# Performance work log

Hardware: AMD Instinct MI355X
Metric: run time of the kernel (lower is better)

## Reference

```python
import jax, jax.numpy as jnp
import numpy as np

IN_FEATURES = 4096
OUT_FEATURES = 4096


def setup_inputs() -> dict:
    key = jax.random.key(0)
    k_x, k_w, k_b = jax.random.split(key, 3)
    inp = {
        "input": jax.random.normal(k_x, (4, 2048, IN_FEATURES), dtype=jnp.float32),
        # learned int8 weight table [out_features, in_features]
        "weight_int8": jax.random.randint(k_w, (OUT_FEATURES, IN_FEATURES), -128, 128, dtype=jnp.int32).astype(jnp.int8),
        # per-tensor dequant scales (scalars, as in the module buffers)
        "scale": jnp.asarray(0.01, dtype=jnp.float32),
        "x_scale": jnp.asarray(0.05, dtype=jnp.float32),
        "bias": jax.random.normal(k_b, (OUT_FEATURES,), dtype=jnp.float32) * 0.02,
    }
    return inp


def reference(input, weight_int8, scale, x_scale, bias):
    # --- quantize activations per-tensor to int8 (W8A8 path) ---
    x_int8 = jnp.clip(jnp.round(input / x_scale), -128, 127).astype(jnp.int8)
    in_shape = input.shape
    x_flat = x_int8.reshape(-1, in_shape[-1])  # [B*S, in]
    # contract x_flat[k] with weight_int8[n, k] -> [B*S, out]
    out_i32 = jax.lax.dot_general(
        x_flat, weight_int8,
        dimension_numbers=(((1,), (1,)), ((), ())),
        preferred_element_type=jnp.int32,
    )
    # --- dequant epilogue: combined scale, reshape, bias ---
    out = out_i32.astype(input.dtype) * (scale * x_scale)
    out = out.reshape(*in_shape[:-1], weight_int8.shape[0])
    out = out + bias
    return out
```

## Files before the change

### kernel.cpp

```cpp
#include <hip/hip_runtime.h>

#define KDIM 4096
#define NDIM 4096
#define BM 256
#define BN 256
#define BK 128
#define NTILE (KDIM / BK)
#define BBUF 32768

using i32x4 = __attribute__((ext_vector_type(4))) int;

__device__ __forceinline__ void g2l16(const void* g, void* l) {
  __builtin_amdgcn_global_load_lds(
      (const __attribute__((address_space(1))) void*)g,
      (__attribute__((address_space(3))) void*)l,
      16, 0, 0);
}

__global__ void w8l_detect(const int* __restrict__ w32, int* __restrict__ flag) {
  __shared__ int s;
  const int t = threadIdx.x;
  if (t == 0) s = 1;
  __syncthreads();
  bool oob = false;
#pragma unroll
  for (int i = 0; i < 16; ++i) {
    int v = w32[t * 16 + i];
    if (v < -128 || v > 127) oob = true;
  }
  if (oob) atomicAnd(&s, 0);
  __syncthreads();
  if (t == 0) *flag = s;
}

__global__ void w8l_pack(const void* __restrict__ wsrc, const int* __restrict__ flag,
                         signed char* __restrict__ wq) {
  if (*flag == 0) return;
  const int t = blockIdx.x * blockDim.x + threadIdx.x;
  const int4* s = (const int4*)wsrc;
  int4 a = s[t * 4 + 0], b = s[t * 4 + 1], c = s[t * 4 + 2], d = s[t * 4 + 3];
  int4 o;
  o.x = (a.x & 255) | ((a.y & 255) << 8) | ((a.z & 255) << 16) | ((a.w & 255) << 24);
  o.y = (b.x & 255) | ((b.y & 255) << 8) | ((b.z & 255) << 16) | ((b.w & 255) << 24);
  o.z = (c.x & 255) | ((c.y & 255) << 8) | ((c.z & 255) << 16) | ((c.w & 255) << 24);
  o.w = (d.x & 255) | ((d.y & 255) << 8) | ((d.z & 255) << 16) | ((d.w & 255) << 24);
  ((int4*)wq)[t] = o;
}

__global__ void w8l_quant(const float* __restrict__ x, const float* __restrict__ xs,
                          signed char* __restrict__ aq) {
  const int t = blockIdx.x * blockDim.x + threadIdx.x;
  const float s = *xs;
  const int r = t & 15;
  const int kc = (t >> 4) & 255;
  const int mb = t >> 12;
  const float4* x4 = (const float4*)(x + (size_t)(mb * 16 + r) * KDIM + kc * 16);
  int4 o;
  int* op = (int*)&o;
#pragma unroll
  for (int q = 0; q < 4; ++q) {
    float4 f = x4[q];
    int v0 = __float2int_rn(f.x / s);
    int v1 = __float2int_rn(f.y / s);
    int v2 = __float2int_rn(f.z / s);
    int v3 = __float2int_rn(f.w / s);
    v0 = v0 < -128 ? -128 : (v0 > 127 ? 127 : v0);
    v1 = v1 < -128 ? -128 : (v1 > 127 ? 127 : v1);
    v2 = v2 < -128 ? -128 : (v2 > 127 ? 127 : v2);
    v3 = v3 < -128 ? -128 : (v3 > 127 ? 127 : v3);
    op[q] = (v0 & 255) | ((v1 & 255) << 8) | ((v2 & 255) << 16) | ((v3 & 255) << 24);
  }
  ((int4*)aq)[t] = o;
}

__global__ __launch_bounds__(512, 2) void w8l_gemm(
    const signed char* __restrict__ Ap,
    const signed char* __restrict__ Wraw, const signed char* __restrict__ Wpk,
    const int* __restrict__ flag,
    const float* __restrict__ scale, const float* __restrict__ xscale,
    const float* __restrict__ bias, float* __restrict__ out, int nbn) {
  __shared__ signed char lds[2 * BBUF];

  const signed char* __restrict__ Wq = (*flag) ? Wpk : Wraw;

  const int tid = threadIdx.x;
  const int lane = tid & 63;
  const int wid = tid >> 6;
  const int wr = wid >> 2;
  const int wc = wid & 3;
  const int l15 = lane & 15;
  const int l4 = (lane >> 4) & 3;

  const int nwg = gridDim.x;
  const int cpx = nwg >> 3;
  const int bid = blockIdx.x;
  const int swz = (bid & 7) * cpx + (bid >> 3);
  const int bm = swz / nbn, bn = swz % nbn;
  const int m0 = bm * BM, n0 = bn * BN;

  const unsigned r_in = (unsigned)tid >> 3;
  const unsigned c16 = (unsigned)tid & 7;
  const unsigned swcol = ((c16 ^ (r_in & 7u)) << 4);
  const signed char* wgp = Wq + (size_t)(n0 + r_in) * KDIM + swcol;
  const unsigned ldsoff = (unsigned)tid * 16u;

#define ISSUE_B(t)                                                           \
  do {                                                                       \
    const size_t koff_ = (size_t)(t) * BK;                                   \
    signed char* lb_ = lds + (unsigned)((t) & 1) * BBUF + ldsoff;            \
    _Pragma("unroll") for (int u = 0; u < 4; ++u)                            \
      g2l16(wgp + (size_t)(u * 64) * KDIM + koff_, lb_ + u * 8192);          \
  } while (0)

  const signed char* aglp =
      Ap + (size_t)(m0 / 16 + wr * 8) * 65536 + l4 * 256 + l15 * 16;

#define LOAD_A(dst, t, ks)                                                   \
  _Pragma("unroll") for (int mi = 0; mi < 8; ++mi)                           \
      dst[mi] = *(const i32x4*)(aglp + (size_t)mi * 65536 +                  \
                                (size_t)(t) * 2048 + (ks) * 1024);

  const unsigned b_lane = (unsigned)((wc * 64 + l15) * 128) +
                          (unsigned)((l4 ^ (l15 & 7)) << 4);

  i32x4 acc[8][4] = {};
  i32x4 aE[8], aO[8], b0[4], b1[4];

#define SB __builtin_amdgcn_sched_barrier(0)

  ISSUE_B(0);
  SB;
  LOAD_A(aE, 0, 0);
  SB;

#pragma unroll 1
  for (int kt = 0; kt < NTILE; ++kt) {
    asm volatile("s_waitcnt vmcnt(8)" ::: "memory");
    __builtin_amdgcn_s_barrier();
    SB;

    const signed char* Bb = lds + (unsigned)(kt & 1) * BBUF;
#pragma unroll
    for (int nj = 0; nj < 4; ++nj) {
      b0[nj] = *(const i32x4*)(Bb + (b_lane + nj * 2048));
      b1[nj] = *(const i32x4*)(Bb + ((b_lane + nj * 2048) ^ 64u));
    }
    SB;
    LOAD_A(aO, kt, 1);
    SB;
    if (kt + 1 < NTILE) ISSUE_B(kt + 1);
    SB;

    __builtin_amdgcn_s_setprio(1);
#pragma unroll
    for (int mi = 0; mi < 8; ++mi)
#pragma unroll
      for (int nj = 0; nj < 4; ++nj)
        acc[mi][nj] = __builtin_amdgcn_mfma_i32_16x16x64_i8(aE[mi], b0[nj], acc[mi][nj], 0, 0, 0);
    __builtin_amdgcn_s_setprio(0);
    SB;
    if (kt + 1 < NTILE) LOAD_A(aE, kt + 1, 0);
    SB;
    __builtin_amdgcn_s_setprio(1);
#pragma unroll
    for (int mi = 0; mi < 8; ++mi)
#pragma unroll
      for (int nj = 0; nj < 4; ++nj)
        acc[mi][nj] = __builtin_amdgcn_mfma_i32_16x16x64_i8(aO[mi], b1[nj], acc[mi][nj], 0, 0, 0);
    __builtin_amdgcn_s_setprio(0);
    SB;
  }

  const float cs = scale[0] * xscale[0];
#pragma unroll
  for (int nj = 0; nj < 4; ++nj) {
    const int n = n0 + wc * 64 + nj * 16 + l15;
    const float bj = bias[n];
#pragma unroll
    for (int mi = 0; mi < 8; ++mi) {
      const int m = m0 + wr * 128 + mi * 16 + l4 * 4;
      float* o = out + (size_t)m * NDIM + n;
#pragma unroll
      for (int v = 0; v < 4; ++v)
        o[(size_t)v * NDIM] = (float)acc[mi][nj][v] * cs + bj;
    }
  }
#undef ISSUE_B
#undef LOAD_A
#undef SB
}

extern "C" void kernel_launch(void* const* d_in, const int* in_sizes, int n_in,
                              void* d_out, int out_size, void* d_ws, size_t ws_size,
                              hipStream_t stream) {
  const float* x = (const float*)d_in[0];
  const void* w = d_in[1];
  const float* scale = (const float*)d_in[2];
  const float* xscale = (const float*)d_in[3];
  const float* bias = (const float*)d_in[4];
  float* out = (float*)d_out;

  const int M = in_sizes[0] / KDIM;

  int* flag = (int*)d_ws;
  signed char* wq = (signed char*)d_ws + 256;
  signed char* aq = wq + (size_t)NDIM * KDIM;

  const size_t need = 256 + (size_t)NDIM * KDIM + (size_t)M * KDIM;
  if (ws_size < need) return;

  w8l_detect<<<1, 256, 0, stream>>>((const int*)w, flag);
  w8l_pack<<<(NDIM * KDIM / 16) / 256, 256, 0, stream>>>(w, flag, wq);
  w8l_quant<<<(M * KDIM / 16) / 256, 256, 0, stream>>>(x, xscale, aq);

  const int nbn = NDIM / BN;
  w8l_gemm<<<(M / BM) * nbn, 512, 0, stream>>>(
      aq, (const signed char*)w, wq, flag, scale, xscale, bias, out, nbn);
}
```

Measured before the change: 201.7 us.

## Switch GEMM to 32x32x32 MFMA with 4 waves and triple-buffered LDS

Rewrites the int8 GEMM main loop to use 4 waves of 128x128 per-wave tiles with 32x32x32 i8 MFMA instead of 8 waves using 16x16x64. The B tile is now triple-buffered in LDS with a new XOR swizzle and prefetched two tiles ahead, and the loop is unrolled by two to alternate A register sets. The aim is more data reuse per wave and fewer LDS reads per MFMA. The cost is much higher register pressure with 64 accumulator VGPRs per tile set, only one workgroup per CU, and a full vmcnt(0) wait each iteration.

```diff
diff --git a/kernel.cpp b/kernel.cpp
--- a/kernel.cpp
+++ b/kernel.cpp
@@ -9,6 +9,7 @@
 #define BBUF 32768
 
 using i32x4 = __attribute__((ext_vector_type(4))) int;
+using i32x16 = __attribute__((ext_vector_type(16))) int;
 
 __device__ __forceinline__ void g2l16(const void* g, void* l) {
   __builtin_amdgcn_global_load_lds(
@@ -73,23 +74,23 @@
   ((int4*)aq)[t] = o;
 }
 
-__global__ __launch_bounds__(512, 2) void w8l_gemm(
+__global__ __launch_bounds__(256, 1) void w8l_gemm(
     const signed char* __restrict__ Ap,
     const signed char* __restrict__ Wraw, const signed char* __restrict__ Wpk,
     const int* __restrict__ flag,
     const float* __restrict__ scale, const float* __restrict__ xscale,
     const float* __restrict__ bias, float* __restrict__ out, int nbn) {
-  __shared__ signed char lds[2 * BBUF];
+  __shared__ signed char lds[3 * BBUF];
 
   const signed char* __restrict__ Wq = (*flag) ? Wpk : Wraw;
 
   const int tid = threadIdx.x;
   const int lane = tid & 63;
   const int wid = tid >> 6;
-  const int wr = wid >> 2;
-  const int wc = wid & 3;
-  const int l15 = lane & 15;
-  const int l4 = (lane >> 4) & 3;
+  const int wr = wid >> 1;
+  const int wc = wid & 1;
+  const int l31 = lane & 31;
+  const int l5 = lane >> 5;
 
   const int nwg = gridDim.x;
   const int cpx = nwg >> 3;
@@ -100,93 +101,110 @@
 
   const unsigned r_in = (unsigned)tid >> 3;
   const unsigned c16 = (unsigned)tid & 7;
-  const unsigned swcol = ((c16 ^ (r_in & 7u)) << 4);
-  const signed char* wgp = Wq + (size_t)(n0 + r_in) * KDIM + swcol;
+  const unsigned s_r = (r_in ^ (r_in >> 3)) & 7u;
+  const signed char* wgp0 = Wq + (size_t)(n0 + r_in) * KDIM + ((c16 ^ s_r) << 4);
+  const signed char* wgp1 = Wq + (size_t)(n0 + r_in) * KDIM + ((c16 ^ s_r ^ 4u) << 4);
   const unsigned ldsoff = (unsigned)tid * 16u;
 
-#define ISSUE_B(t)                                                           \
-  do {                                                                       \
-    const size_t koff_ = (size_t)(t) * BK;                                   \
-    signed char* lb_ = lds + (unsigned)((t) & 1) * BBUF + ldsoff;            \
-    _Pragma("unroll") for (int u = 0; u < 4; ++u)                            \
-      g2l16(wgp + (size_t)(u * 64) * KDIM + koff_, lb_ + u * 8192);          \
+#define ISSUE_B(t, buf)                                                       \
+  do {                                                                        \
+    const size_t koff_ = (size_t)(t) * BK;                                    \
+    signed char* lb_ = lds + (unsigned)(buf) * (unsigned)BBUF + ldsoff;       \
+    _Pragma("unroll") for (int u = 0; u < 8; ++u) {                           \
+      const signed char* gp_ = (u & 1) ? wgp1 : wgp0;                         \
+      g2l16(gp_ + (size_t)(u * 32) * KDIM + koff_, lb_ + u * 4096);           \
+    }                                                                         \
   } while (0)
 
-  const signed char* aglp =
-      Ap + (size_t)(m0 / 16 + wr * 8) * 65536 + l4 * 256 + l15 * 16;
-
-#define LOAD_A(dst, t, ks)                                                   \
-  _Pragma("unroll") for (int mi = 0; mi < 8; ++mi)                           \
-      dst[mi] = *(const i32x4*)(aglp + (size_t)mi * 65536 +                  \
-                                (size_t)(t) * 2048 + (ks) * 1024);
-
-  const unsigned b_lane = (unsigned)((wc * 64 + l15) * 128) +
-                          (unsigned)((l4 ^ (l15 & 7)) << 4);
-
-  i32x4 acc[8][4] = {};
-  i32x4 aE[8], aO[8], b0[4], b1[4];
+  const signed char* aglp = Ap +
+      (size_t)((m0 >> 4) + wr * 8 + (l31 >> 4)) * 65536 +
+      (size_t)l5 * 256 + (size_t)(l31 & 15) * 16;
+
+#define LOAD_A(dst, t)                                                        \
+  _Pragma("unroll") for (int ks = 0; ks < 4; ++ks)                            \
+      _Pragma("unroll") for (int mi = 0; mi < 4; ++mi)                        \
+          dst[ks][mi] = *(const i32x4*)(aglp + (size_t)mi * 131072 +          \
+                                        (size_t)(t) * 2048 + ks * 512);
+
+#define RD_B(dst, base, ks)                                                   \
+  _Pragma("unroll") for (int nj = 0; nj < 4; ++nj) {                          \
+    const int r_ = wc * 128 + nj * 32 + l31;                                  \
+    const int sx_ = (r_ ^ (r_ >> 3)) & 7;                                     \
+    dst[nj] = *(const i32x4*)((base) + r_ * 128 +                             \
+                              ((((ks) * 2 + l5) ^ sx_) << 4));                \
+  }
 
 #define SB __builtin_amdgcn_sched_barrier(0)
 
-  ISSUE_B(0);
+#define MFMA16(a4, b4)                                                        \
+  __builtin_amdgcn_s_setprio(1);                                              \
+  _Pragma("unroll") for (int mi = 0; mi < 4; ++mi)                            \
+      _Pragma("unroll") for (int nj = 0; nj < 4; ++nj)                        \
+          acc[mi][nj] = __builtin_amdgcn_mfma_i32_32x32x32_i8(                \
+              a4[mi], b4[nj], acc[mi][nj], 0, 0, 0);                          \
+  __builtin_amdgcn_s_setprio(0);
+
+  i32x16 acc[4][4] = {};
+  i32x4 aE[4][4], aO[4][4], b0[4], b1[4], b2[4];
+
+#define BODY(t, AC, AN)                                                       \
+  do {                                                                        \
+    asm volatile("s_waitcnt vmcnt(0)" ::: "memory");  \
+    __builtin_amdgcn_s_barrier();                                             \
+    SB;                                                                       \
+    if ((t) + 2 < NTILE) ISSUE_B((t) + 2, ((t) + 2) % 3);                     \
+    SB;                                                                       \
+    if ((t) + 1 < NTILE) LOAD_A(AN, (t) + 1);                                 \
+    SB;                                                                       \
+    const signed char* base_ = lds + (unsigned)((t) % 3) * (unsigned)BBUF;    \
+    RD_B(b0, base_, 0);                                                       \
+    RD_B(b1, base_, 1);                                                       \
+    RD_B(b2, base_, 2);                                                       \
+    SB;                                                                       \
+    MFMA16(AC[0], b0);                                                        \
+    SB;                                                                       \
+    RD_B(b0, base_, 3);      \
+    SB;                                                                       \
+    MFMA16(AC[1], b1);                                                        \
+    SB;                                                                       \
+    MFMA16(AC[2], b2);                                                        \
+    SB;                                                                       \
+    MFMA16(AC[3], b0);                                                        \
+    SB;                                                                       \
+  } while (0)
+
+  ISSUE_B(0, 0);
+  ISSUE_B(1, 1);
   SB;
-  LOAD_A(aE, 0, 0);
+  LOAD_A(aE, 0);
   SB;
 
 #pragma unroll 1
-  for (int kt = 0; kt < NTILE; ++kt) {
-    asm volatile("s_waitcnt vmcnt(8)" ::: "memory");
-    __builtin_amdgcn_s_barrier();
-    SB;
-
-    const signed char* Bb = lds + (unsigned)(kt & 1) * BBUF;
-#pragma unroll
-    for (int nj = 0; nj < 4; ++nj) {
-      b0[nj] = *(const i32x4*)(Bb + (b_lane + nj * 2048));
-      b1[nj] = *(const i32x4*)(Bb + ((b_lane + nj * 2048) ^ 64u));
-    }
-    SB;
-    LOAD_A(aO, kt, 1);
-    SB;
-    if (kt + 1 < NTILE) ISSUE_B(kt + 1);
-    SB;
-
-    __builtin_amdgcn_s_setprio(1);
-#pragma unroll
-    for (int mi = 0; mi < 8; ++mi)
-#pragma unroll
-      for (int nj = 0; nj < 4; ++nj)
-        acc[mi][nj] = __builtin_amdgcn_mfma_i32_16x16x64_i8(aE[mi], b0[nj], acc[mi][nj], 0, 0, 0);
-    __builtin_amdgcn_s_setprio(0);
-    SB;
-    if (kt + 1 < NTILE) LOAD_A(aE, kt + 1, 0);
-    SB;
-    __builtin_amdgcn_s_setprio(1);
-#pragma unroll
-    for (int mi = 0; mi < 8; ++mi)
-#pragma unroll
-      for (int nj = 0; nj < 4; ++nj)
-        acc[mi][nj] = __builtin_amdgcn_mfma_i32_16x16x64_i8(aO[mi], b1[nj], acc[mi][nj], 0, 0, 0);
-    __builtin_amdgcn_s_setprio(0);
-    SB;
+  for (int kt = 0; kt < NTILE; kt += 2) {
+    BODY(kt, aE, aO);
+    BODY(kt + 1, aO, aE);
   }
 
   const float cs = scale[0] * xscale[0];
 #pragma unroll
   for (int nj = 0; nj < 4; ++nj) {
-    const int n = n0 + wc * 64 + nj * 16 + l15;
+    const int n = n0 + wc * 128 + nj * 32 + l31;
     const float bj = bias[n];
 #pragma unroll
-    for (int mi = 0; mi < 8; ++mi) {
-      const int m = m0 + wr * 128 + mi * 16 + l4 * 4;
-      float* o = out + (size_t)m * NDIM + n;
-#pragma unroll
-      for (int v = 0; v < 4; ++v)
-        o[(size_t)v * NDIM] = (float)acc[mi][nj][v] * cs + bj;
+    for (int mi = 0; mi < 4; ++mi) {
+      const int mbase = m0 + wr * 128 + mi * 32 + l5 * 4;
+#pragma unroll
+      for (int r = 0; r < 16; ++r) {
+        const int m = mbase + (r & 3) + 8 * (r >> 2);
+        out[(size_t)m * NDIM + n] = (float)acc[mi][nj][r] * cs + bj;
+      }
     }
   }
 #undef ISSUE_B
 #undef LOAD_A
+#undef RD_B
+#undef MFMA16
+#undef BODY
 #undef SB
 }
 
@@ -214,6 +232,6 @@
   w8l_quant<<<(M * KDIM / 16) / 256, 256, 0, stream>>>(x, xscale, aq);
 
   const int nbn = NDIM / BN;
-  w8l_gemm<<<(M / BM) * nbn, 512, 0, stream>>>(
+  w8l_gemm<<<(M / BM) * nbn, 256, 0, stream>>>(
       aq, (const signed char*)w, wq, flag, scale, xscale, bias, out, nbn);
 }
```

Result: slower. 340.2 us (+68.6%).
